# Kernel optimization log

Measured on AMD Instinct MI355X. Metric: run time of the kernel, lower is better.

Reference implementation:

```python
import jax, jax.numpy as jnp
import numpy as np

B, H, L = 32, 512, 2          # batch, hidden_dim, n_rnn layers per tier
F0 = 128                      # top-tier frame count
UPS = (2, 8)                  # up-sampling factors for tiers 0 and 1
FRAMES = (F0, F0 * UPS[0], F0 * UPS[0] * UPS[1])


def setup_inputs() -> dict:
    key = jax.random.key(0)
    ks = iter(jax.random.split(key, 64))
    k = 1.0 / np.sqrt(H)
    u = lambda shape: jax.random.uniform(next(ks), shape, jnp.float32, -k, k)
    inp = {}
    for t in range(3):
        inp[f"x{t}"] = jax.random.normal(next(ks), (B, FRAMES[t], H), jnp.float32)
    for t in range(3):
        inp[f"Wih{t}"] = u((L, 4 * H, H))
        inp[f"Whh{t}"] = u((L, 4 * H, H))
        inp[f"bih{t}"] = u((L, 4 * H))
        inp[f"bhh{t}"] = u((L, 4 * H))
        inp[f"h0_{t}"] = jax.random.normal(next(ks), (L, B, H), jnp.float32)
        inp[f"c0_{t}"] = jax.random.normal(next(ks), (L, B, H), jnp.float32)
    inp["upW0"] = u((H, UPS[0] * H)); inp["upb0"] = u((UPS[0] * H,))
    inp["upW1"] = u((H, UPS[1] * H)); inp["upb1"] = u((UPS[1] * H,))
    return inp


def _lstm(x, Wih, Whh, bih, bhh, h0, c0):
    # x: (B,T,H); Wih/Whh: (L,4H,H); torch gate order i,f,g,o
    for l in range(L):
        xg = jnp.einsum('bth,gh->btg', x, Wih[l]) + bih[l]  # (B,T,4H)
        Whh_l, bhh_l = Whh[l], bhh[l]

        def step(carry, g_t):
            h, c = carry
            g = g_t + h @ Whh_l.T + bhh_l
            i, f, gg, o = jnp.split(g, 4, axis=-1)
            c = jax.nn.sigmoid(f) * c + jax.nn.sigmoid(i) * jnp.tanh(gg)
            h = jax.nn.sigmoid(o) * jnp.tanh(c)
            return (h, c), h

        _, hs = jax.lax.scan(step, (h0[l], c0[l]), jnp.swapaxes(xg, 0, 1))
        x = jnp.swapaxes(hs, 0, 1)
    return x


def _upsample(x, W, b, t):
    # LinearResampler: Linear(H -> t*H) then unfold time: (B,T,H)->(B,T*t,H)
    Bx, T, Hx = x.shape
    y = x @ W + b  # (B,T,t*H)
    return y.reshape(Bx, T * t, Hx)


def reference(x0, x1, x2,
              Wih0, Whh0, bih0, bhh0, h0_0, c0_0,
              Wih1, Whh1, bih1, bhh1, h0_1, c0_1,
              Wih2, Whh2, bih2, bhh2, h0_2, c0_2,
              upW0, upb0, upW1, upb1):
    h = _lstm(x0, Wih0, Whh0, bih0, bhh0, h0_0, c0_0)
    h = _upsample(h, upW0, upb0, UPS[0])
    h = _lstm(x1 + h, Wih1, Whh1, bih1, bhh1, h0_1, c0_1)
    h = _upsample(h, upW1, upb1, UPS[1])
    h = _lstm(x2 + h, Wih2, Whh2, bih2, bhh2, h0_2, c0_2)
    return h
```

## Files before the change

kernel.cpp:

```cpp
#include <hip/hip_runtime.h>
#include <cstddef>
#include <cstdint>

#define NB 32
#define HD 512
#define GD 2048
#define NL0 32
#define NL1 64
#define FSTR 64
#define NSLOT 8
#define LOSC 0.00048828125f

typedef unsigned short u16;
typedef unsigned int u32;
typedef unsigned long long u64;
typedef _Float16 f16;
typedef __attribute__((ext_vector_type(8))) _Float16 f16x8;
typedef __attribute__((ext_vector_type(4))) float f32x4;

#define MFMAF(a, b, c) __builtin_amdgcn_mfma_f32_16x16x32_f16((a), (b), (c), 0, 0, 0)
#define AT_LD(p)   __hip_atomic_load((p), __ATOMIC_RELAXED, __HIP_MEMORY_SCOPE_AGENT)

#define LDG16(dst, p) \
    asm volatile("global_load_dwordx4 %0, %1, off sc0 sc1" : "=&v"(dst) : "v"(p))
#define ST8(p, v) \
    asm volatile("global_store_dwordx2 %0, %1, off sc0 sc1" :: "v"(p), "v"(v) : "memory")
#define VMCNT0() asm volatile("s_waitcnt vmcnt(0)" ::: "memory")
#define SBAR()   __builtin_amdgcn_sched_barrier(0)

__device__ __forceinline__ float sigf(float x)   { return 1.0f / (1.0f + __expf(-x)); }
__device__ __forceinline__ float tanhf_(float x) { return 2.0f / (1.0f + __expf(-2.0f * x)) - 1.0f; }

__device__ __forceinline__ u16 f2h_bits(float x) {
    f16 h = (f16)x; union { f16 f; u16 u; } c; c.f = h; return c.u;
}
__device__ __forceinline__ float h2f(u16 b) {
    union { u16 u; f16 f; } c; c.u = b; return (float)c.f;
}

__device__ __forceinline__ void split8f(const float4 a, const float4 b, f16x8& hi, f16x8& lo) {
    float v[8] = {a.x, a.y, a.z, a.w, b.x, b.y, b.z, b.w};
#pragma unroll
    for (int q = 0; q < 8; ++q) {
        const f16 h = (f16)v[q];
        hi[q] = h;
        lo[q] = (f16)((v[q] - (float)h) * 2048.0f);
    }
}
__device__ __forceinline__ void cvt8(const float4 a, const float4 b, f16x8& o) {
    o[0] = (f16)a.x; o[1] = (f16)a.y; o[2] = (f16)a.z; o[3] = (f16)a.w;
    o[4] = (f16)b.x; o[5] = (f16)b.y; o[6] = (f16)b.z; o[7] = (f16)b.w;
}

__global__ __launch_bounds__(256) void wsplit_kernel(
    const float* __restrict__ src, u16* __restrict__ hi, u16* __restrict__ lo, int n)
{
    const int i = blockIdx.x * 256 + threadIdx.x;
    if (i < n) {
        const float x = src[i];
        const f16 h = (f16)x;
        union { f16 f; u16 u; } c; c.f = h;
        hi[i] = c.u;
        lo[i] = f2h_bits((x - (float)h) * 2048.0f);
    }
}

__global__ __launch_bounds__(256) void cvtf_kernel(
    const float* __restrict__ src, u16* __restrict__ dst, int n)
{
    const int i = blockIdx.x * 256 + threadIdx.x;
    if (i < n) dst[i] = f2h_bits(src[i]);
}

__global__ __launch_bounds__(256) void addv_kernel(
    const float* __restrict__ a, const float* __restrict__ b, float* __restrict__ o, int n)
{
    const int i = blockIdx.x * 256 + threadIdx.x;
    if (i < n) o[i] = a[i] + b[i];
}

template<int MODE>
__global__ __launch_bounds__(256) void mfma_gemm(
    const float* __restrict__ A, int T, int t0, int tc_bits,
    const float* __restrict__ W, int N,
    const float* __restrict__ b1, const float* __restrict__ b2x,
    float* __restrict__ out, int t_bits, int u_bits)
{
    __shared__ __align__(16) u16 As[64][40], Bh[64][40], Bl[64][40];
    const int tid = threadIdx.x;
    const int m0 = blockIdx.x << 6, n0 = blockIdx.y << 6;

    const int ar = tid >> 2, aks = (tid & 3) << 3;
    const float* aPtr;
    if (MODE == 0) {
        const int rg = m0 + ar;
        const int b = rg >> tc_bits;
        const int tt = t0 + (rg & ((1 << tc_bits) - 1));
        aPtr = A + (((size_t)b * T + tt) << 9) + aks;
    } else {
        aPtr = A + (((size_t)(m0 + ar)) << 9) + aks;
    }
    const float* bPtr = nullptr;
    int bkk = 0, bns = 0;
    if (MODE == 0) {
        bPtr = W + (((size_t)(n0 + ar)) << 9) + aks;
    } else {
        bkk = tid >> 3; bns = (tid & 7) << 3;
        bPtr = W + (size_t)bkk * N + n0 + bns;
    }

    const int lane = tid & 63, wv = tid >> 6;
    const int fr = lane & 15, ko = (lane >> 4) << 3;
    f32x4 acc[4] = {}, accl[4] = {};

    for (int k0 = 0; k0 < HD; k0 += 32) {
        {
            const float4 a1 = *(const float4*)(aPtr + k0);
            const float4 a2 = *(const float4*)(aPtr + k0 + 4);
            f16x8 av; cvt8(a1, a2, av);
            *(f16x8*)&As[ar][aks] = av;
        }
        if (MODE == 0) {
            const float4 w1 = *(const float4*)(bPtr + k0);
            const float4 w2 = *(const float4*)(bPtr + k0 + 4);
            f16x8 vh, vl; split8f(w1, w2, vh, vl);
            *(f16x8*)&Bh[ar][aks] = vh;
            *(f16x8*)&Bl[ar][aks] = vl;
        } else {
            const float4 w1 = *(const float4*)(bPtr + (size_t)k0 * N);
            const float4 w2 = *(const float4*)(bPtr + (size_t)k0 * N + 4);
            f16x8 vh, vl; split8f(w1, w2, vh, vl);
#pragma unroll
            for (int q = 0; q < 8; ++q) {
                union { f16 f; u16 u; } ch, cl; ch.f = vh[q]; cl.f = vl[q];
                Bh[bns + q][bkk] = ch.u;
                Bl[bns + q][bkk] = cl.u;
            }
        }
        __syncthreads();
        const f16x8 ahf = *(const f16x8*)&As[(wv << 4) + fr][ko];
#pragma unroll
        for (int nt = 0; nt < 4; ++nt) {
            const f16x8 bhf = *(const f16x8*)&Bh[(nt << 4) + fr][ko];
            const f16x8 blf = *(const f16x8*)&Bl[(nt << 4) + fr][ko];
            acc[nt]  = MFMAF(ahf, bhf, acc[nt]);
            accl[nt] = MFMAF(ahf, blf, accl[nt]);
        }
        __syncthreads();
    }

    const int mlb = (wv << 4) + ((lane >> 4) << 2);
#pragma unroll
    for (int r = 0; r < 4; ++r) {
        const int mg = m0 + mlb + r;
#pragma unroll
        for (int nt = 0; nt < 4; ++nt) {
            const int n = n0 + (nt << 4) + fr;
            const float v = acc[nt][r] + accl[nt][r] * LOSC;
            if (MODE == 0) {
                out[((size_t)mg << 11) + n] = v + b1[n] + b2x[n];
            } else {
                const int bb = mg >> t_bits, tt = mg & ((1 << t_bits) - 1);
                const int uu = n >> 9, hh = n & 511;
                const size_t di = (((size_t)((((bb << t_bits) + tt) << u_bits) + uu)) << 9) + hh;
                out[di] = v + b1[n] + b2x[di];
            }
        }
    }
}


#define SPIN_WAIT(TGT0, TGT1) do { \
    if (tid < NL0 + NL1) { \
        const int tgt_ = (tid < NL0) ? (TGT0) : (TGT1); \
        if (tgt_ > 0) { \
            const u32* fp_ = flags + tid * FSTR; \
            int g_ = 0; \
            while ((int)AT_LD(fp_) < tgt_ && ++g_ < (1 << 24)) {} \
        } \
    } \
    SBAR(); \
    __syncthreads(); \
} while (0)

__global__ __launch_bounds__(512, 2) void lstm_scan8(
    const float* __restrict__ xg, int Tc,
    const u16* __restrict__ w0h,
    const u16* __restrict__ w1ih_h,
    const u16* __restrict__ w1hh_h,
    const float* __restrict__ bsum1,
    u16* __restrict__ r0, u16* __restrict__ r1,
    float* __restrict__ c0ws, float* __restrict__ c1ws,
    float* __restrict__ out1, int T, int t0, int NS,
    u32* __restrict__ flags)
{
    __shared__ __align__(16) float sred[16 * 32 * 20];
    __shared__ u16 spk[16][33];
    const int tid = threadIdx.x;
    const int bid = blockIdx.x;
    const int lane = tid & 63, wv = tid >> 6;
    const int kq = wv >> 1, bh = wv & 1;
    const int fr = lane & 15, kg = lane >> 4;
    const int batch = (bh << 4) + fr;
    const int eb = tid & 31;
    const u32 bko = ((u32)batch << 9) + (kq << 7) + (kg << 3);

    if (bid < NL0) {
        const int j0 = bid << 4;
        f16x8 Ah_[16];
#pragma unroll
        for (int hq = 0; hq < 4; ++hq) {
            const size_t grow = (((size_t)(fr & 3)) << 9) + j0 + (hq << 2) + (fr >> 2);
#pragma unroll
            for (int ck = 0; ck < 4; ++ck)
                Ah_[(hq << 2) | ck] = *(const f16x8*)(
                    w0h + (grow << 9) + (kq << 7) + (ck << 5) + (kg << 3));
        }
        const int eh = tid >> 5;
        const int hidden = j0 + eh;
        float c_reg = c0ws[((size_t)eb << 9) + hidden];
        __syncthreads();

        for (int jj = 0; jj < Tc; ++jj) {
            const int t = t0 + jj;
            float xv[4];
#pragma unroll
            for (int g = 0; g < 4; ++g)
                xv[g] = xg[(((size_t)eb * Tc + jj) << 11) + (g << 9) + hidden];
            SPIN_WAIT(jj, jj - 6);
            const u16* bp = r0 + (((size_t)((t - 1) & 7)) << 14) + bko;
            f16x8 vb[4];
#pragma unroll
            for (int ck = 0; ck < 4; ++ck)
                LDG16(vb[ck], bp + (ck << 5));
            f32x4 s0[4] = {};
            VMCNT0(); SBAR();
#pragma unroll
            for (int hq = 0; hq < 4; ++hq)
#pragma unroll
                for (int ck = 0; ck < 4; ++ck)
                    s0[hq] = MFMAF(Ah_[(hq << 2) | ck], vb[ck], s0[hq]);
#pragma unroll
            for (int hq = 0; hq < 4; ++hq) {
                const int h16 = (hq << 2) + kg;
                *(f32x4*)&sred[((h16 << 5) + batch) * 20 + (kq << 2)] = s0[hq];
            }
            __syncthreads();
            {
                const int base = ((eh << 5) + eb) * 20;
                const f32x4 q0 = *(const f32x4*)&sred[base];
                const f32x4 q1 = *(const f32x4*)&sred[base + 4];
                const f32x4 q2 = *(const f32x4*)&sred[base + 8];
                const f32x4 q3 = *(const f32x4*)&sred[base + 12];
                const float gi = q0[0] + q1[0] + q2[0] + q3[0] + xv[0];
                const float gf = q0[1] + q1[1] + q2[1] + q3[1] + xv[1];
                const float gg = q0[2] + q1[2] + q2[2] + q3[2] + xv[2];
                const float go = q0[3] + q1[3] + q2[3] + q3[3] + xv[3];
                c_reg = sigf(gf) * c_reg + sigf(gi) * tanhf_(gg);
                const float h = sigf(go) * tanhf_(c_reg);
                spk[eh][eb] = f2h_bits(h);
            }
            __syncthreads();
            if (tid < 128) {
                const int bt = tid & 31, h4 = (tid >> 5) << 2;
                const u64 hp = (u64)spk[h4 + 0][bt] | ((u64)spk[h4 + 1][bt] << 16)
                             | ((u64)spk[h4 + 2][bt] << 32) | ((u64)spk[h4 + 3][bt] << 48);
                const size_t wo = (((size_t)(t & 7)) << 14) + ((size_t)bt << 9) + j0 + h4;
                ST8(r0 + wo, hp);
            }
            VMCNT0();
            __syncthreads();
            if (tid == 0)
                __hip_atomic_store(flags + bid * FSTR, (u32)(jj + 1),
                                   __ATOMIC_RELAXED, __HIP_MEMORY_SCOPE_AGENT);
        }
        c0ws[((size_t)eb << 9) + hidden] = c_reg;
    } else {
        const int j0 = (bid - NL0) << 3;
        f16x8 Ah_[16];
#pragma unroll
        for (int mat = 0; mat < 2; ++mat)
#pragma unroll
            for (int hq = 0; hq < 2; ++hq) {
                const size_t grow = (((size_t)(fr & 3)) << 9) + j0 + (hq << 2) + (fr >> 2);
                const u16* src = mat ? w1hh_h : w1ih_h;
#pragma unroll
                for (int ck = 0; ck < 4; ++ck)
                    Ah_[(((mat << 1) | hq) << 2) | ck] = *(const f16x8*)(
                        src + (grow << 9) + (kq << 7) + (ck << 5) + (kg << 3));
            }
        const int eh = tid >> 5;
        const int hidden = j0 + (eh & 7);
        float bs[4], c_reg = 0.f;
        if (tid < 256) {
#pragma unroll
            for (int g = 0; g < 4; ++g) bs[g] = bsum1[(g << 9) + hidden];
            c_reg = c1ws[((size_t)eb << 9) + hidden];
        }
        __syncthreads();

        for (int jj = 0; jj < NS; ++jj) {
            const int t = t0 + jj - 1;
            SPIN_WAIT(jj, jj);
            if (t >= 0) {
                const u16* ap = r0 + (((size_t)(t & 7)) << 14) + bko;
                const u16* bp = r1 + (((size_t)((t - 1) & 7)) << 14) + bko;
                f16x8 va[4], vb[4];
#pragma unroll
                for (int ck = 0; ck < 4; ++ck) {
                    LDG16(va[ck], ap + (ck << 5));
                    LDG16(vb[ck], bp + (ck << 5));
                }
                f32x4 s0[2] = {};
                VMCNT0(); SBAR();
#pragma unroll
                for (int hq = 0; hq < 2; ++hq)
#pragma unroll
                    for (int ck = 0; ck < 4; ++ck) {
                        const int ia = (hq << 2) | ck;
                        const int ib = ((2 + hq) << 2) | ck;
                        s0[hq] = MFMAF(Ah_[ia], va[ck], s0[hq]);
                        s0[hq] = MFMAF(Ah_[ib], vb[ck], s0[hq]);
                    }
#pragma unroll
                for (int hq = 0; hq < 2; ++hq) {
                    const int h8 = (hq << 2) + kg;
                    *(f32x4*)&sred[((h8 << 5) + batch) * 20 + (kq << 2)] = s0[hq];
                }
            }
            __syncthreads();
            if (t >= 0 && tid < 256) {
                const int base = ((eh << 5) + eb) * 20;
                const f32x4 q0 = *(const f32x4*)&sred[base];
                const f32x4 q1 = *(const f32x4*)&sred[base + 4];
                const f32x4 q2 = *(const f32x4*)&sred[base + 8];
                const f32x4 q3 = *(const f32x4*)&sred[base + 12];
                const float gi = q0[0] + q1[0] + q2[0] + q3[0] + bs[0];
                const float gf = q0[1] + q1[1] + q2[1] + q3[1] + bs[1];
                const float gg = q0[2] + q1[2] + q2[2] + q3[2] + bs[2];
                const float go = q0[3] + q1[3] + q2[3] + q3[3] + bs[3];
                c_reg = sigf(gf) * c_reg + sigf(gi) * tanhf_(gg);
                const float h = sigf(go) * tanhf_(c_reg);
                spk[eh][eb] = f2h_bits(h);
            }
            __syncthreads();
            if (t >= 0 && tid < 64) {
                const int bt = tid & 31, h4 = (tid >> 5) << 2;
                const u64 hp = (u64)spk[h4 + 0][bt] | ((u64)spk[h4 + 1][bt] << 16)
                             | ((u64)spk[h4 + 2][bt] << 32) | ((u64)spk[h4 + 3][bt] << 48);
                const size_t wo = (((size_t)(t & 7)) << 14) + ((size_t)bt << 9) + j0 + h4;
                ST8(r1 + wo, hp);
            }
            VMCNT0();
            __syncthreads();
            if (tid == 0)
                __hip_atomic_store(flags + bid * FSTR, (u32)(jj + 1),
                                   __ATOMIC_RELAXED, __HIP_MEMORY_SCOPE_AGENT);
            if (t >= 0 && tid < 64) {
                const int bt = tid & 31, h4 = (tid >> 5) << 2;
                float4 o;
                o.x = h2f(spk[h4 + 0][bt]);
                o.y = h2f(spk[h4 + 1][bt]);
                o.z = h2f(spk[h4 + 2][bt]);
                o.w = h2f(spk[h4 + 3][bt]);
                *(float4*)(out1 + (((size_t)bt * T + t) << 9) + j0 + h4) = o;
            }
        }
        if (tid < 256) c1ws[((size_t)eb << 9) + hidden] = c_reg;
    }
}

extern "C" void kernel_launch(void* const* d_in, const int* in_sizes, int n_in,
                              void* d_out, int out_size, void* d_ws, size_t ws_size,
                              hipStream_t stream)
{
    const float* x[3]   = {(const float*)d_in[0], (const float*)d_in[1],  (const float*)d_in[2]};
    const float* Wih[3] = {(const float*)d_in[3], (const float*)d_in[9],  (const float*)d_in[15]};
    const float* Whh[3] = {(const float*)d_in[4], (const float*)d_in[10], (const float*)d_in[16]};
    const float* bih[3] = {(const float*)d_in[5], (const float*)d_in[11], (const float*)d_in[17]};
    const float* bhh[3] = {(const float*)d_in[6], (const float*)d_in[12], (const float*)d_in[18]};
    const float* h0[3]  = {(const float*)d_in[7], (const float*)d_in[13], (const float*)d_in[19]};
    const float* c0[3]  = {(const float*)d_in[8], (const float*)d_in[14], (const float*)d_in[20]};
    const float* upW[2] = {(const float*)d_in[21], (const float*)d_in[23]};
    const float* upb[2] = {(const float*)d_in[22], (const float*)d_in[24]};

    float* ws = (float*)d_ws;
    float* bufA  = ws;
    float* bufB  = bufA + (size_t)NB * 256 * HD;
    float* c0ws  = bufB + (size_t)NB * 256 * HD;
    float* c1ws  = c0ws + (size_t)NB * HD;
    float* bsum1 = c1ws + (size_t)NB * HD;
    float* xg    = bsum1 + GD;

    const size_t head_f = 2 * (size_t)NB * 256 * HD + 2 * (size_t)NB * HD + GD;
    const size_t tail_f = 3 * (size_t)GD * HD + NSLOT * (size_t)NB * HD + 96 * FSTR + 64;
    int Tc_cap = 512;
    while (Tc_cap > 32 && (head_f + (size_t)NB * Tc_cap * GD + tail_f) * 4 > ws_size)
        Tc_cap >>= 1;

    u16* w0h    = (u16*)(xg + (size_t)NB * Tc_cap * GD);
    u16* w0l    = w0h + (size_t)GD * HD;
    u16* w1ih_h = w0l + (size_t)GD * HD;
    u16* w1ih_l = w1ih_h + (size_t)GD * HD;
    u16* w1hh_h = w1ih_l + (size_t)GD * HD;
    u16* w1hh_l = w1hh_h + (size_t)GD * HD;
    u16* r0     = w1hh_l + (size_t)GD * HD;
    u16* r1     = r0 + NSLOT * (size_t)NB * HD;
    u32* flags  = (u32*)(r1 + NSLOT * (size_t)NB * HD);

    auto tier = [&](const float* in, float* out1, int T, int tr) {
        const float* Wih0L = Wih[tr];
        const float* Whh0L = Whh[tr];
        const float* Wih1L = Wih[tr] + (size_t)GD * HD;
        const float* Whh1L = Whh[tr] + (size_t)GD * HD;

        wsplit_kernel<<<(GD * HD) / 256, 256, 0, stream>>>(Whh0L, w0h, w0l, GD * HD);
        wsplit_kernel<<<(GD * HD) / 256, 256, 0, stream>>>(Wih1L, w1ih_h, w1ih_l, GD * HD);
        wsplit_kernel<<<(GD * HD) / 256, 256, 0, stream>>>(Whh1L, w1hh_h, w1hh_l, GD * HD);
        addv_kernel<<<GD / 256, 256, 0, stream>>>(bih[tr] + GD, bhh[tr] + GD, bsum1, GD);
        cvtf_kernel<<<(NB * HD) / 256, 256, 0, stream>>>(
            h0[tr], r0 + 7 * (size_t)NB * HD, NB * HD);
        cvtf_kernel<<<(NB * HD) / 256, 256, 0, stream>>>(
            h0[tr] + (size_t)NB * HD, r1 + 7 * (size_t)NB * HD, NB * HD);
        hipMemcpyAsync(c0ws, c0[tr], (size_t)NB * HD * sizeof(float),
                       hipMemcpyDeviceToDevice, stream);
        hipMemcpyAsync(c1ws, c0[tr] + (size_t)NB * HD, (size_t)NB * HD * sizeof(float),
                       hipMemcpyDeviceToDevice, stream);

        const int Tc = T < Tc_cap ? T : Tc_cap;
        int tc_bits = 0; while ((1 << tc_bits) < Tc) ++tc_bits;
        for (int t0 = 0; t0 < T; t0 += Tc) {
            dim3 g((NB * Tc) / 64, GD / 64);
            mfma_gemm<0><<<g, 256, 0, stream>>>(in, T, t0, tc_bits, Wih0L, GD,
                                                bih[tr], bhh[tr], xg, 0, 0);
            hipMemsetAsync(flags, 0, 96 * FSTR * sizeof(u32), stream);
            const bool last = (t0 + Tc >= T);
            const int NS = Tc + (last ? 1 : 0);
            const float* xg_p = xg; int Tc_a = Tc;
            const u16 *a0 = w0h, *a2 = w1ih_h, *a4 = w1hh_h;
            const float* bs_p = bsum1;
            u16 *p0 = r0, *p1 = r1;
            float *c0p = c0ws, *c1p = c1ws, *o1 = out1;
            int T_a = T, t0_a = t0, NS_a = NS;
            u32* fl = flags;
            void* args[] = {(void*)&xg_p, (void*)&Tc_a,
                            (void*)&a0, (void*)&a2, (void*)&a4,
                            (void*)&bs_p, (void*)&p0, (void*)&p1,
                            (void*)&c0p, (void*)&c1p, (void*)&o1,
                            (void*)&T_a, (void*)&t0_a, (void*)&NS_a, (void*)&fl};
            hipLaunchCooperativeKernel((const void*)lstm_scan8, dim3(NL0 + NL1), dim3(512),
                                       args, 0, stream);
        }
    };

    float* dout = (float*)d_out;

    tier(x[0], bufB, 128, 0);
    {
        dim3 g((NB * 128) / 64, 1024 / 64);
        mfma_gemm<1><<<g, 256, 0, stream>>>(bufB, 0, 0, 0, upW[0], 1024,
                                            upb[0], x[1], bufA, 7, 1);
    }
    tier(bufA, bufB, 256, 1);
    {
        dim3 g((NB * 256) / 64, 4096 / 64);
        mfma_gemm<1><<<g, 256, 0, stream>>>(bufB, 0, 0, 0, upW[1], 4096,
                                            upb[1], x[2], dout, 8, 3);
    }
    tier(dout, dout, 2048, 2);
}
```

Measured before the change: 10.64 ms.

## Repartition LSTM scan so each wave owns full K, dropping LDS reduction

```diff
diff --git a/kernel.cpp b/kernel.cpp
--- a/kernel.cpp
+++ b/kernel.cpp
@@ -50,19 +50,6 @@
 __device__ __forceinline__ void cvt8(const float4 a, const float4 b, f16x8& o) {
     o[0] = (f16)a.x; o[1] = (f16)a.y; o[2] = (f16)a.z; o[3] = (f16)a.w;
     o[4] = (f16)b.x; o[5] = (f16)b.y; o[6] = (f16)b.z; o[7] = (f16)b.w;
-}
-
-__global__ __launch_bounds__(256) void wsplit_kernel(
-    const float* __restrict__ src, u16* __restrict__ hi, u16* __restrict__ lo, int n)
-{
-    const int i = blockIdx.x * 256 + threadIdx.x;
-    if (i < n) {
-        const float x = src[i];
-        const f16 h = (f16)x;
-        union { f16 f; u16 u; } c; c.f = h;
-        hi[i] = c.u;
-        lo[i] = f2h_bits((x - (float)h) * 2048.0f);
-    }
 }
 
 __global__ __launch_bounds__(256) void cvtf_kernel(
@@ -183,7 +170,7 @@
     __syncthreads(); \
 } while (0)
 
-__global__ __launch_bounds__(512, 2) void lstm_scan8(
+__global__ __launch_bounds__(512, 1) void lstm_scan9(
     const float* __restrict__ xg, int Tc,
     const u16* __restrict__ w0h,
     const u16* __restrict__ w1ih_h,
@@ -194,31 +181,26 @@
     float* __restrict__ out1, int T, int t0, int NS,
     u32* __restrict__ flags)
 {
-    __shared__ __align__(16) float sred[16 * 32 * 20];
+    __shared__ __align__(16) float cmb[4][64][4];
     __shared__ u16 spk[16][33];
     const int tid = threadIdx.x;
     const int bid = blockIdx.x;
     const int lane = tid & 63, wv = tid >> 6;
-    const int kq = wv >> 1, bh = wv & 1;
     const int fr = lane & 15, kg = lane >> 4;
-    const int batch = (bh << 4) + fr;
-    const int eb = tid & 31;
-    const u32 bko = ((u32)batch << 9) + (kq << 7) + (kg << 3);
 
     if (bid < NL0) {
         const int j0 = bid << 4;
+        const int hq = wv >> 1, bh = wv & 1;
+        const int jq = j0 + (hq << 2);
+        const int batch = (bh << 4) + fr;
+        const int hidden = jq + kg;
+        const size_t arow = (((size_t)(fr & 3)) << 9) + jq + (fr >> 2);
         f16x8 Ah_[16];
 #pragma unroll
-        for (int hq = 0; hq < 4; ++hq) {
-            const size_t grow = (((size_t)(fr & 3)) << 9) + j0 + (hq << 2) + (fr >> 2);
-#pragma unroll
-            for (int ck = 0; ck < 4; ++ck)
-                Ah_[(hq << 2) | ck] = *(const f16x8*)(
-                    w0h + (grow << 9) + (kq << 7) + (ck << 5) + (kg << 3));
-        }
-        const int eh = tid >> 5;
-        const int hidden = j0 + eh;
-        float c_reg = c0ws[((size_t)eb << 9) + hidden];
+        for (int ck = 0; ck < 16; ++ck)
+            Ah_[ck] = *(const f16x8*)(w0h + (arow << 9) + (ck << 5) + (kg << 3));
+        float c_reg = c0ws[((size_t)batch << 9) + hidden];
+        const u32 bko = ((u32)batch << 9) + (kg << 3);
         __syncthreads();
 
         for (int jj = 0; jj < Tc; ++jj) {
@@ -226,40 +208,28 @@
             float xv[4];
 #pragma unroll
             for (int g = 0; g < 4; ++g)
-                xv[g] = xg[(((size_t)eb * Tc + jj) << 11) + (g << 9) + hidden];
+                xv[g] = xg[(((size_t)batch * Tc + jj) << 11) + (g << 9) + hidden];
             SPIN_WAIT(jj, jj - 6);
             const u16* bp = r0 + (((size_t)((t - 1) & 7)) << 14) + bko;
-            f16x8 vb[4];
-#pragma unroll
-            for (int ck = 0; ck < 4; ++ck)
+            f16x8 vb[16];
+#pragma unroll
+            for (int ck = 0; ck < 16; ++ck)
                 LDG16(vb[ck], bp + (ck << 5));
-            f32x4 s0[4] = {};
+            f32x4 sa = {}, sb = {};
             VMCNT0(); SBAR();
 #pragma unroll
-            for (int hq = 0; hq < 4; ++hq)
-#pragma unroll
-                for (int ck = 0; ck < 4; ++ck)
-                    s0[hq] = MFMAF(Ah_[(hq << 2) | ck], vb[ck], s0[hq]);
-#pragma unroll
-            for (int hq = 0; hq < 4; ++hq) {
-                const int h16 = (hq << 2) + kg;
-                *(f32x4*)&sred[((h16 << 5) + batch) * 20 + (kq << 2)] = s0[hq];
-            }
-            __syncthreads();
-            {
-                const int base = ((eh << 5) + eb) * 20;
-                const f32x4 q0 = *(const f32x4*)&sred[base];
-                const f32x4 q1 = *(const f32x4*)&sred[base + 4];
-                const f32x4 q2 = *(const f32x4*)&sred[base + 8];
-                const f32x4 q3 = *(const f32x4*)&sred[base + 12];
-                const float gi = q0[0] + q1[0] + q2[0] + q3[0] + xv[0];
-                const float gf = q0[1] + q1[1] + q2[1] + q3[1] + xv[1];
-                const float gg = q0[2] + q1[2] + q2[2] + q3[2] + xv[2];
-                const float go = q0[3] + q1[3] + q2[3] + q3[3] + xv[3];
-                c_reg = sigf(gf) * c_reg + sigf(gi) * tanhf_(gg);
-                const float h = sigf(go) * tanhf_(c_reg);
-                spk[eh][eb] = f2h_bits(h);
-            }
+            for (int ck = 0; ck < 16; ck += 2) {
+                sa = MFMAF(Ah_[ck], vb[ck], sa);
+                sb = MFMAF(Ah_[ck + 1], vb[ck + 1], sb);
+            }
+            const f32x4 s = sa + sb;
+            const float gi = s[0] + xv[0];
+            const float gf = s[1] + xv[1];
+            const float gg = s[2] + xv[2];
+            const float go = s[3] + xv[3];
+            c_reg = sigf(gf) * c_reg + sigf(gi) * tanhf_(gg);
+            const float h = sigf(go) * tanhf_(c_reg);
+            spk[(hq << 2) + kg][batch] = f2h_bits(h);
             __syncthreads();
             if (tid < 128) {
                 const int bt = tid & 31, h4 = (tid >> 5) << 2;
@@ -274,74 +244,58 @@
                 __hip_atomic_store(flags + bid * FSTR, (u32)(jj + 1),
                                    __ATOMIC_RELAXED, __HIP_MEMORY_SCOPE_AGENT);
         }
-        c0ws[((size_t)eb << 9) + hidden] = c_reg;
+        c0ws[((size_t)batch << 9) + hidden] = c_reg;
     } else {
         const int j0 = (bid - NL0) << 3;
+        const int m = wv >> 2, hq = (wv >> 1) & 1, bh = wv & 1;
+        const int jq = j0 + (hq << 2);
+        const int batch = (bh << 4) + fr;
+        const int hidden = jq + kg;
+        const int pr = wv & 3;
+        const size_t arow = (((size_t)(fr & 3)) << 9) + jq + (fr >> 2);
+        const u16* Wsrc = m ? w1hh_h : w1ih_h;
         f16x8 Ah_[16];
 #pragma unroll
-        for (int mat = 0; mat < 2; ++mat)
-#pragma unroll
-            for (int hq = 0; hq < 2; ++hq) {
-                const size_t grow = (((size_t)(fr & 3)) << 9) + j0 + (hq << 2) + (fr >> 2);
-                const u16* src = mat ? w1hh_h : w1ih_h;
-#pragma unroll
-                for (int ck = 0; ck < 4; ++ck)
-                    Ah_[(((mat << 1) | hq) << 2) | ck] = *(const f16x8*)(
-                        src + (grow << 9) + (kq << 7) + (ck << 5) + (kg << 3));
-            }
-        const int eh = tid >> 5;
-        const int hidden = j0 + (eh & 7);
-        float bs[4], c_reg = 0.f;
-        if (tid < 256) {
-#pragma unroll
-            for (int g = 0; g < 4; ++g) bs[g] = bsum1[(g << 9) + hidden];
-            c_reg = c1ws[((size_t)eb << 9) + hidden];
-        }
+        for (int ck = 0; ck < 16; ++ck)
+            Ah_[ck] = *(const f16x8*)(Wsrc + (arow << 9) + (ck << 5) + (kg << 3));
+        float bs[4];
+#pragma unroll
+        for (int g = 0; g < 4; ++g) bs[g] = bsum1[(g << 9) + hidden];
+        float c_reg = c1ws[((size_t)batch << 9) + hidden];
+        const u32 bko = ((u32)batch << 9) + (kg << 3);
         __syncthreads();
 
         for (int jj = 0; jj < NS; ++jj) {
             const int t = t0 + jj - 1;
             SPIN_WAIT(jj, jj);
+            f32x4 s = {};
             if (t >= 0) {
-                const u16* ap = r0 + (((size_t)(t & 7)) << 14) + bko;
-                const u16* bp = r1 + (((size_t)((t - 1) & 7)) << 14) + bko;
-                f16x8 va[4], vb[4];
-#pragma unroll
-                for (int ck = 0; ck < 4; ++ck) {
-                    LDG16(va[ck], ap + (ck << 5));
+                const u16* bp = m ? (r1 + (((size_t)((t - 1) & 7)) << 14) + bko)
+                                  : (r0 + (((size_t)(t & 7)) << 14) + bko);
+                f16x8 vb[16];
+#pragma unroll
+                for (int ck = 0; ck < 16; ++ck)
                     LDG16(vb[ck], bp + (ck << 5));
+                f32x4 sa = {}, sb = {};
+                VMCNT0(); SBAR();
+#pragma unroll
+                for (int ck = 0; ck < 16; ck += 2) {
+                    sa = MFMAF(Ah_[ck], vb[ck], sa);
+                    sb = MFMAF(Ah_[ck + 1], vb[ck + 1], sb);
                 }
-                f32x4 s0[2] = {};
-                VMCNT0(); SBAR();
-#pragma unroll
-                for (int hq = 0; hq < 2; ++hq)
-#pragma unroll
-                    for (int ck = 0; ck < 4; ++ck) {
-                        const int ia = (hq << 2) | ck;
-                        const int ib = ((2 + hq) << 2) | ck;
-                        s0[hq] = MFMAF(Ah_[ia], va[ck], s0[hq]);
-                        s0[hq] = MFMAF(Ah_[ib], vb[ck], s0[hq]);
-                    }
-#pragma unroll
-                for (int hq = 0; hq < 2; ++hq) {
-                    const int h8 = (hq << 2) + kg;
-                    *(f32x4*)&sred[((h8 << 5) + batch) * 20 + (kq << 2)] = s0[hq];
-                }
+                s = sa + sb;
+                if (m) *(f32x4*)&cmb[pr][lane][0] = s;
             }
             __syncthreads();
-            if (t >= 0 && tid < 256) {
-                const int base = ((eh << 5) + eb) * 20;
-                const f32x4 q0 = *(const f32x4*)&sred[base];
-                const f32x4 q1 = *(const f32x4*)&sred[base + 4];
-                const f32x4 q2 = *(const f32x4*)&sred[base + 8];
-                const f32x4 q3 = *(const f32x4*)&sred[base + 12];
-                const float gi = q0[0] + q1[0] + q2[0] + q3[0] + bs[0];
-                const float gf = q0[1] + q1[1] + q2[1] + q3[1] + bs[1];
-                const float gg = q0[2] + q1[2] + q2[2] + q3[2] + bs[2];
-                const float go = q0[3] + q1[3] + q2[3] + q3[3] + bs[3];
+            if (t >= 0 && m == 0) {
+                const f32x4 o = *(const f32x4*)&cmb[pr][lane][0];
+                const float gi = s[0] + o[0] + bs[0];
+                const float gf = s[1] + o[1] + bs[1];
+                const float gg = s[2] + o[2] + bs[2];
+                const float go = s[3] + o[3] + bs[3];
                 c_reg = sigf(gf) * c_reg + sigf(gi) * tanhf_(gg);
                 const float h = sigf(go) * tanhf_(c_reg);
-                spk[eh][eb] = f2h_bits(h);
+                spk[(hq << 2) + kg][batch] = f2h_bits(h);
             }
             __syncthreads();
             if (t >= 0 && tid < 64) {
@@ -366,7 +320,7 @@
                 *(float4*)(out1 + (((size_t)bt * T + t) << 9) + j0 + h4) = o;
             }
         }
-        if (tid < 256) c1ws[((size_t)eb << 9) + hidden] = c_reg;
+        if (m == 0) c1ws[((size_t)batch << 9) + hidden] = c_reg;
     }
 }
 
@@ -393,18 +347,15 @@
     float* xg    = bsum1 + GD;
 
     const size_t head_f = 2 * (size_t)NB * 256 * HD + 2 * (size_t)NB * HD + GD;
-    const size_t tail_f = 3 * (size_t)GD * HD + NSLOT * (size_t)NB * HD + 96 * FSTR + 64;
-    int Tc_cap = 512;
+    const size_t tail_f = 3 * (size_t)GD * HD / 2 + NSLOT * (size_t)NB * HD + 96 * FSTR + 64;
+    int Tc_cap = 1024;
     while (Tc_cap > 32 && (head_f + (size_t)NB * Tc_cap * GD + tail_f) * 4 > ws_size)
         Tc_cap >>= 1;
 
     u16* w0h    = (u16*)(xg + (size_t)NB * Tc_cap * GD);
-    u16* w0l    = w0h + (size_t)GD * HD;
-    u16* w1ih_h = w0l + (size_t)GD * HD;
-    u16* w1ih_l = w1ih_h + (size_t)GD * HD;
-    u16* w1hh_h = w1ih_l + (size_t)GD * HD;
-    u16* w1hh_l = w1hh_h + (size_t)GD * HD;
-    u16* r0     = w1hh_l + (size_t)GD * HD;
+    u16* w1ih_h = w0h + (size_t)GD * HD;
+    u16* w1hh_h = w1ih_h + (size_t)GD * HD;
+    u16* r0     = w1hh_h + (size_t)GD * HD;
     u16* r1     = r0 + NSLOT * (size_t)NB * HD;
     u32* flags  = (u32*)(r1 + NSLOT * (size_t)NB * HD);
 
@@ -414,9 +365,9 @@
         const float* Wih1L = Wih[tr] + (size_t)GD * HD;
         const float* Whh1L = Whh[tr] + (size_t)GD * HD;
 
-        wsplit_kernel<<<(GD * HD) / 256, 256, 0, stream>>>(Whh0L, w0h, w0l, GD * HD);
-        wsplit_kernel<<<(GD * HD) / 256, 256, 0, stream>>>(Wih1L, w1ih_h, w1ih_l, GD * HD);
-        wsplit_kernel<<<(GD * HD) / 256, 256, 0, stream>>>(Whh1L, w1hh_h, w1hh_l, GD * HD);
+        cvtf_kernel<<<(GD * HD) / 256, 256, 0, stream>>>(Whh0L, w0h, GD * HD);
+        cvtf_kernel<<<(GD * HD) / 256, 256, 0, stream>>>(Wih1L, w1ih_h, GD * HD);
+        cvtf_kernel<<<(GD * HD) / 256, 256, 0, stream>>>(Whh1L, w1hh_h, GD * HD);
         addv_kernel<<<GD / 256, 256, 0, stream>>>(bih[tr] + GD, bhh[tr] + GD, bsum1, GD);
         cvtf_kernel<<<(NB * HD) / 256, 256, 0, stream>>>(
             h0[tr], r0 + 7 * (size_t)NB * HD, NB * HD);
@@ -448,7 +399,7 @@
                             (void*)&bs_p, (void*)&p0, (void*)&p1,
                             (void*)&c0p, (void*)&c1p, (void*)&o1,
                             (void*)&T_a, (void*)&t0_a, (void*)&NS_a, (void*)&fl};
-            hipLaunchCooperativeKernel((const void*)lstm_scan8, dim3(NL0 + NL1), dim3(512),
+            hipLaunchCooperativeKernel((const void*)lstm_scan9, dim3(NL0 + NL1), dim3(512),
                                        args, 0, stream);
         }
     };
```

After: 15.80 ms. 48.6% more time.

## Overlap next chunk's input-gate GEMM with LSTM scan using extra cooperative blocks

Applied to the files above, without the earlier changes.

```diff
diff --git a/kernel.cpp b/kernel.cpp
--- a/kernel.cpp
+++ b/kernel.cpp
@@ -7,6 +7,7 @@
 #define GD 2048
 #define NL0 32
 #define NL1 64
+#define NGB 160
 #define FSTR 64
 #define NSLOT 8
 #define LOSC 0.00048828125f
@@ -183,7 +184,7 @@
     __syncthreads(); \
 } while (0)
 
-__global__ __launch_bounds__(512, 2) void lstm_scan8(
+__global__ __launch_bounds__(512, 2) void lstm_scan8f(
     const float* __restrict__ xg, int Tc,
     const u16* __restrict__ w0h,
     const u16* __restrict__ w1ih_h,
@@ -192,10 +193,15 @@
     u16* __restrict__ r0, u16* __restrict__ r1,
     float* __restrict__ c0ws, float* __restrict__ c1ws,
     float* __restrict__ out1, int T, int t0, int NS,
-    u32* __restrict__ flags)
+    u32* __restrict__ flags,
+    const float* __restrict__ gA, int gt0, int gtc_bits,
+    const float* __restrict__ gW,
+    const float* __restrict__ gb1, const float* __restrict__ gb2x,
+    float* __restrict__ gxg, int ntiles, int mtiles)
 {
     __shared__ __align__(16) float sred[16 * 32 * 20];
     __shared__ u16 spk[16][33];
+    __shared__ __align__(16) u16 gAs[64][40], gBh[64][40], gBl[64][40];
     const int tid = threadIdx.x;
     const int bid = blockIdx.x;
     const int lane = tid & 63, wv = tid >> 6;
@@ -275,7 +281,7 @@
                                    __ATOMIC_RELAXED, __HIP_MEMORY_SCOPE_AGENT);
         }
         c0ws[((size_t)eb << 9) + hidden] = c_reg;
-    } else {
+    } else if (bid < NL0 + NL1) {
         const int j0 = (bid - NL0) << 3;
         f16x8 Ah_[16];
 #pragma unroll
@@ -354,7 +360,7 @@
             VMCNT0();
             __syncthreads();
             if (tid == 0)
-                __hip_atomic_store(flags + bid * FSTR, (u32)(jj + 1),
+                __hip_atomic_store(flags + (bid) * FSTR, (u32)(jj + 1),
                                    __ATOMIC_RELAXED, __HIP_MEMORY_SCOPE_AGENT);
             if (t >= 0 && tid < 64) {
                 const int bt = tid & 31, h4 = (tid >> 5) << 2;
@@ -367,6 +373,63 @@
             }
         }
         if (tid < 256) c1ws[((size_t)eb << 9) + hidden] = c_reg;
+    } else {
+        const int gb = bid - (NL0 + NL1);
+        const int ko = kg << 3;
+        for (int tile = gb; tile < ntiles; tile += NGB) {
+            const int m0 = (tile % mtiles) << 6;
+            const int n0 = (tile / mtiles) << 6;
+            const int ar = tid >> 2, aks = (tid & 3) << 3;
+            const float* aPtr = nullptr;
+            const float* bPtr = nullptr;
+            if (tid < 256) {
+                const int rg = m0 + ar;
+                const int b = rg >> gtc_bits;
+                const int tt = gt0 + (rg & ((1 << gtc_bits) - 1));
+                aPtr = gA + (((size_t)b * T + tt) << 9) + aks;
+                bPtr = gW + (((size_t)(n0 + ar)) << 9) + aks;
+            }
+            const int wv4 = (tid >> 6) & 3;
+            f32x4 acc[4] = {}, accl[4] = {};
+            for (int k0 = 0; k0 < HD; k0 += 32) {
+                if (tid < 256) {
+                    const float4 a1 = *(const float4*)(aPtr + k0);
+                    const float4 a2 = *(const float4*)(aPtr + k0 + 4);
+                    f16x8 av; cvt8(a1, a2, av);
+                    *(f16x8*)&gAs[ar][aks] = av;
+                    const float4 w1 = *(const float4*)(bPtr + k0);
+                    const float4 w2 = *(const float4*)(bPtr + k0 + 4);
+                    f16x8 vh, vl; split8f(w1, w2, vh, vl);
+                    *(f16x8*)&gBh[ar][aks] = vh;
+                    *(f16x8*)&gBl[ar][aks] = vl;
+                }
+                __syncthreads();
+                if (tid < 256) {
+                    const f16x8 ahf = *(const f16x8*)&gAs[(wv4 << 4) + fr][ko];
+#pragma unroll
+                    for (int nt = 0; nt < 4; ++nt) {
+                        const f16x8 bhf = *(const f16x8*)&gBh[(nt << 4) + fr][ko];
+                        const f16x8 blf = *(const f16x8*)&gBl[(nt << 4) + fr][ko];
+                        acc[nt]  = MFMAF(ahf, bhf, acc[nt]);
+                        accl[nt] = MFMAF(ahf, blf, accl[nt]);
+                    }
+                }
+                __syncthreads();
+            }
+            if (tid < 256) {
+                const int mlb = (wv4 << 4) + (kg << 2);
+#pragma unroll
+                for (int r = 0; r < 4; ++r) {
+                    const int mg = m0 + mlb + r;
+#pragma unroll
+                    for (int nt = 0; nt < 4; ++nt) {
+                        const int n = n0 + (nt << 4) + fr;
+                        gxg[((size_t)mg << 11) + n] =
+                            acc[nt][r] + accl[nt][r] * LOSC + gb1[n] + gb2x[n];
+                    }
+                }
+            }
+        }
     }
 }
 
@@ -390,15 +453,16 @@
     float* c0ws  = bufB + (size_t)NB * 256 * HD;
     float* c1ws  = c0ws + (size_t)NB * HD;
     float* bsum1 = c1ws + (size_t)NB * HD;
-    float* xg    = bsum1 + GD;
+    float* xgA   = bsum1 + GD;
 
     const size_t head_f = 2 * (size_t)NB * 256 * HD + 2 * (size_t)NB * HD + GD;
     const size_t tail_f = 3 * (size_t)GD * HD + NSLOT * (size_t)NB * HD + 96 * FSTR + 64;
     int Tc_cap = 512;
-    while (Tc_cap > 32 && (head_f + (size_t)NB * Tc_cap * GD + tail_f) * 4 > ws_size)
+    while (Tc_cap > 32 && (head_f + 2 * (size_t)NB * Tc_cap * GD + tail_f) * 4 > ws_size)
         Tc_cap >>= 1;
 
-    u16* w0h    = (u16*)(xg + (size_t)NB * Tc_cap * GD);
+    float* xgB  = xgA + (size_t)NB * Tc_cap * GD;
+    u16* w0h    = (u16*)(xgB + (size_t)NB * Tc_cap * GD);
     u16* w0l    = w0h + (size_t)GD * HD;
     u16* w1ih_h = w0l + (size_t)GD * HD;
     u16* w1ih_l = w1ih_h + (size_t)GD * HD;
@@ -429,26 +493,40 @@
 
         const int Tc = T < Tc_cap ? T : Tc_cap;
         int tc_bits = 0; while ((1 << tc_bits) < Tc) ++tc_bits;
-        for (int t0 = 0; t0 < T; t0 += Tc) {
-            dim3 g((NB * Tc) / 64, GD / 64);
-            mfma_gemm<0><<<g, 256, 0, stream>>>(in, T, t0, tc_bits, Wih0L, GD,
-                                                bih[tr], bhh[tr], xg, 0, 0);
+        const int nchunks = T / Tc;
+        const int mtiles = (NB * Tc) / 64;
+        float* xgb[2] = {xgA, xgB};
+
+        {
+            dim3 g(mtiles, GD / 64);
+            mfma_gemm<0><<<g, 256, 0, stream>>>(in, T, 0, tc_bits, Wih0L, GD,
+                                                bih[tr], bhh[tr], xgb[0], 0, 0);
+        }
+        for (int ci = 0; ci < nchunks; ++ci) {
+            const int t0 = ci * Tc;
             hipMemsetAsync(flags, 0, 96 * FSTR * sizeof(u32), stream);
-            const bool last = (t0 + Tc >= T);
+            const bool last = (ci == nchunks - 1);
             const int NS = Tc + (last ? 1 : 0);
-            const float* xg_p = xg; int Tc_a = Tc;
+            const int ntiles = last ? 0 : mtiles * (GD / 64);
+            const float* xg_p = xgb[ci & 1]; int Tc_a = Tc;
             const u16 *a0 = w0h, *a2 = w1ih_h, *a4 = w1hh_h;
             const float* bs_p = bsum1;
             u16 *p0 = r0, *p1 = r1;
             float *c0p = c0ws, *c1p = c1ws, *o1 = out1;
             int T_a = T, t0_a = t0, NS_a = NS;
             u32* fl = flags;
+            const float* gA = in; int gt0 = t0 + Tc; int gtc = tc_bits;
+            const float* gW = Wih0L; const float* g1 = bih[tr]; const float* g2 = bhh[tr];
+            float* gx = xgb[(ci + 1) & 1]; int nt_a = ntiles; int mt_a = mtiles;
             void* args[] = {(void*)&xg_p, (void*)&Tc_a,
                             (void*)&a0, (void*)&a2, (void*)&a4,
                             (void*)&bs_p, (void*)&p0, (void*)&p1,
                             (void*)&c0p, (void*)&c1p, (void*)&o1,
-                            (void*)&T_a, (void*)&t0_a, (void*)&NS_a, (void*)&fl};
-            hipLaunchCooperativeKernel((const void*)lstm_scan8, dim3(NL0 + NL1), dim3(512),
+                            (void*)&T_a, (void*)&t0_a, (void*)&NS_a, (void*)&fl,
+                            (void*)&gA, (void*)&gt0, (void*)&gtc,
+                            (void*)&gW, (void*)&g1, (void*)&g2,
+                            (void*)&gx, (void*)&nt_a, (void*)&mt_a};
+            hipLaunchCooperativeKernel((const void*)lstm_scan8f, dim3(256), dim3(512),
                                        args, 0, stream);
         }
     };
```

Result: faster. 10.41 ms (median of 2 runs) (-2.1%).
